# Kernel optimization log

Measured on AMD Instinct MI355X. Metric: run time of the kernel, lower is better.

Reference implementation:

```python
import jax, jax.numpy as jnp
import numpy as np
from jax import lax

B, C_IN, IMG, P, HID = 128, 3, 224, 16, 768
HW = (IMG // P) ** 2  # 196 patches


def setup_inputs() -> dict:
    key = jax.random.key(0)
    k1, k2, k3, k4 = jax.random.split(key, 4)
    x = jax.random.normal(k1, (B, C_IN, IMG, IMG), dtype=jnp.float32)
    # conv weight init scale ~ kaiming-ish, value irrelevant for correctness
    W = jax.random.normal(k2, (HID, C_IN, P, P), dtype=jnp.float32) * 0.02
    b = jax.random.normal(k3, (HID,), dtype=jnp.float32) * 0.02
    # per-sample random permutation of patch positions (the pixel shuffle)
    perm = jax.vmap(lambda k: jax.random.permutation(k, HW))(jax.random.split(k4, B)).astype(jnp.int32)
    return {"x": x, "W": W, "b": b, "perm": perm}


def reference(x, W, b, perm):
    # patchify conv: kernel_size == stride == P, no padding
    enc = lax.conv_general_dilated(
        x, W, window_strides=(P, P), padding="VALID",
        dimension_numbers=("NCHW", "OIHW", "NCHW"),
    ) + b[None, :, None, None]                      # [B, HID, H', W']
    Bc, Cc, Hc, Wc = enc.shape
    enc = enc.reshape(Bc, Cc, Hc * Wc).transpose(0, 2, 1)   # [B, HW, HID]
    # per-sample patch shuffle: shuffled[i, j] = enc[i, perm[i, j]]
    shuffled = jnp.take_along_axis(enc, perm[:, :, None], axis=1)
    return shuffled
```

## Files before the change

### kernel.cpp

```cpp
#include <hip/hip_runtime.h>
#include <hip/hip_bf16.h>

#define BATCH  128
#define HWN    196
#define HIDN   768
#define KN     768
#define IMGSZ  224
#define IMG2   (224*224)
#define MTOT   (BATCH*HWN)

#define BM 128
#define BN 128
#define BK 32
#define NBM (MTOT/BM)
#define NBN (HIDN/BN)
#define NWG (NBM*NBN)
#define CPX (NWG/8)

typedef __attribute__((ext_vector_type(8))) short bf16x8;
typedef __attribute__((ext_vector_type(4))) float floatx4;

#define GP(p) ((const __attribute__((address_space(1))) void*)(p))
#define SP(p) ((__attribute__((address_space(3))) void*)(p))

static __device__ __forceinline__ short f2bf(float f) {
    __hip_bfloat16 h = __float2bfloat16(f);
    return __builtin_bit_cast(short, h);
}

static __device__ __forceinline__ bf16x8 cvt8(const float* __restrict__ src) {
    float4 f0 = *(const float4*)(src);
    float4 f1 = *(const float4*)(src + 4);
    bf16x8 v;
    v[0]=f2bf(f0.x); v[1]=f2bf(f0.y); v[2]=f2bf(f0.z); v[3]=f2bf(f0.w);
    v[4]=f2bf(f1.x); v[5]=f2bf(f1.y); v[6]=f2bf(f1.z); v[7]=f2bf(f1.w);
    return v;
}

__global__ __launch_bounds__(256)
void prep_A(const float* __restrict__ x, unsigned short* __restrict__ A)
{
    const int idx = blockIdx.x * 256 + threadIdx.x;
    const int gr  = idx / 48;
    const int seg = idx - gr * 48;
    const int b   = gr / HWN;
    const int p   = gr - b * HWN;
    const int py  = p / 14, px = p - py * 14;
    const int c   = seg >> 4;
    const int iy  = seg & 15;

    const float* src = x + (size_t)b * 3 * IMG2 + (size_t)c * IMG2
                         + (size_t)(py * 16 + iy) * IMGSZ + px * 16;
    bf16x8 v0 = cvt8(src);
    bf16x8 v1 = cvt8(src + 8);
    unsigned short* dst = A + (size_t)gr * KN + seg * 16;
    *(bf16x8*)(dst)     = v0;
    *(bf16x8*)(dst + 8) = v1;
}

__global__ __launch_bounds__(256)
void prep_W(const float* __restrict__ W, unsigned short* __restrict__ Wb)
{
    const int idx = blockIdx.x * 256 + threadIdx.x;
    const float* src = W + (size_t)idx * 8;
    *(bf16x8*)(Wb + (size_t)idx * 8) = cvt8(src);
}

__global__ __launch_bounds__(256, 3)
void gemm(const unsigned short* __restrict__ A, const int* __restrict__ perm,
          const unsigned short* __restrict__ Wb,
          const float* __restrict__ bias, float* __restrict__ out)
{
    __shared__ __align__(16) unsigned short As[BM * BK];
    __shared__ __align__(16) unsigned short Bs[BN * BK];

    const int tid = threadIdx.x;
    const int wg  = blockIdx.x;
    const int lid = (wg & 7) * CPX + (wg >> 3);
    const int bm  = lid / NBN;
    const int bn  = lid - bm * NBN;

    const int srow = tid >> 2;
    const int sseg = tid & 3;
    const int gr0 = bm * BM + srow;
    const int gr1 = gr0 + 64;
    const int b0  = gr0 / HWN;
    const int b1  = gr1 / HWN;
    const int pr0 = b0 * HWN + perm[gr0];
    const int pr1 = b1 * HWN + perm[gr1];
    const unsigned short* ga0 = A  + (size_t)pr0 * KN + sseg * 8;
    const unsigned short* ga1 = A  + (size_t)pr1 * KN + sseg * 8;
    const unsigned short* gb  = Wb + (size_t)(bn * BN + srow) * KN + sseg * 8;

    const int lane = tid & 63;
    const int wave = tid >> 6;
    const int wm = (wave >> 1) * 64;
    const int wn = (wave & 1) * 64;
    const int lr = lane & 15;
    const int lq = lane >> 4;

    floatx4 acc[4][4] = {};

    for (int k0 = 0; k0 < KN; k0 += BK) {
        __builtin_amdgcn_global_load_lds(GP(ga0 + k0),           SP(&As[tid * 8]),        16, 0, 0);
        __builtin_amdgcn_global_load_lds(GP(ga1 + k0),           SP(&As[2048 + tid * 8]), 16, 0, 0);
        __builtin_amdgcn_global_load_lds(GP(gb + k0),            SP(&Bs[tid * 8]),        16, 0, 0);
        __builtin_amdgcn_global_load_lds(GP(gb + 64 * KN + k0),  SP(&Bs[2048 + tid * 8]), 16, 0, 0);
        __syncthreads();

        bf16x8 bfrag[4];
        #pragma unroll
        for (int j = 0; j < 4; ++j)
            bfrag[j] = *(const bf16x8*)&Bs[(wn + j * 16 + lr) * BK + lq * 8];
        #pragma unroll
        for (int i = 0; i < 4; ++i) {
            bf16x8 afrag = *(const bf16x8*)&As[(wm + i * 16 + lr) * BK + lq * 8];
            #pragma unroll
            for (int j = 0; j < 4; ++j)
                acc[i][j] = __builtin_amdgcn_mfma_f32_16x16x32_bf16(
                                afrag, bfrag[j], acc[i][j], 0, 0, 0);
        }
        __syncthreads();
    }

    #pragma unroll
    for (int j = 0; j < 4; ++j) {
        const int gc = bn * BN + wn + j * 16 + lr;
        const float bv = bias[gc];
        #pragma unroll
        for (int i = 0; i < 4; ++i) {
            const int grow = bm * BM + wm + i * 16 + lq * 4;
            float* op = out + (size_t)grow * HIDN + gc;
            #pragma unroll
            for (int r = 0; r < 4; ++r)
                op[(size_t)r * HIDN] = acc[i][j][r] + bv;
        }
    }
}

extern "C" void kernel_launch(void* const* d_in, const int* in_sizes, int n_in,
                              void* d_out, int out_size, void* d_ws, size_t ws_size,
                              hipStream_t stream) {
    const float* x    = (const float*)d_in[0];
    const float* W    = (const float*)d_in[1];
    const float* bias = (const float*)d_in[2];
    const int*   perm = (const int*)d_in[3];
    float* out = (float*)d_out;

    unsigned short* A  = (unsigned short*)d_ws;
    unsigned short* Wb = A + (size_t)MTOT * KN;

    prep_A<<<dim3(MTOT * 48 / 256), dim3(256), 0, stream>>>(x, A);
    prep_W<<<dim3(KN * HIDN / 8 / 256), dim3(256), 0, stream>>>(W, Wb);
    gemm<<<dim3(NWG), dim3(256), 0, stream>>>(A, perm, Wb, bias, out);
}
```

Measured before the change: 182.3 us.

## Double GEMM M-tile to 256 with 512 threads and fuse prep kernels

The GEMM workgroup grows to 512 threads covering a 256x128 output tile. The intent is to halve the number of times each B tile is reloaded and to let eight waves share the LDS-staged operands. The XCD swizzle is rewritten to handle a workgroup count that is not divisible by 8. The two bf16 conversion prep kernels are merged into one launch to save launch overhead. The larger tile leaves fewer workgroups (588) and raises LDS use per block, which may reduce occupancy and load balance.

```diff
diff --git a/kernel.cpp b/kernel.cpp
--- a/kernel.cpp
+++ b/kernel.cpp
@@ -9,13 +9,17 @@
 #define IMG2   (224*224)
 #define MTOT   (BATCH*HWN)
 
-#define BM 128
+#define BM 256
 #define BN 128
 #define BK 32
 #define NBM (MTOT/BM)
 #define NBN (HIDN/BN)
 #define NWG (NBM*NBN)
-#define CPX (NWG/8)
+#define SWQ (NWG/8)
+#define SWR (NWG%8)
+
+#define PWB (KN*HIDN/8/256)
+#define PAB (MTOT*48/256)
 
 typedef __attribute__((ext_vector_type(8))) short bf16x8;
 typedef __attribute__((ext_vector_type(4))) float floatx4;
@@ -38,9 +42,15 @@
 }
 
 __global__ __launch_bounds__(256)
-void prep_A(const float* __restrict__ x, unsigned short* __restrict__ A)
+void prep(const float* __restrict__ x, const float* __restrict__ W,
+          unsigned short* __restrict__ A, unsigned short* __restrict__ Wb)
 {
-    const int idx = blockIdx.x * 256 + threadIdx.x;
+    if (blockIdx.x < PWB) {
+        const int idx = blockIdx.x * 256 + threadIdx.x;
+        *(bf16x8*)(Wb + (size_t)idx * 8) = cvt8(W + (size_t)idx * 8);
+        return;
+    }
+    const int idx = (blockIdx.x - PWB) * 256 + threadIdx.x;
     const int gr  = idx / 48;
     const int seg = idx - gr * 48;
     const int b   = gr / HWN;
@@ -58,15 +68,7 @@
     *(bf16x8*)(dst + 8) = v1;
 }
 
-__global__ __launch_bounds__(256)
-void prep_W(const float* __restrict__ W, unsigned short* __restrict__ Wb)
-{
-    const int idx = blockIdx.x * 256 + threadIdx.x;
-    const float* src = W + (size_t)idx * 8;
-    *(bf16x8*)(Wb + (size_t)idx * 8) = cvt8(src);
-}
-
-__global__ __launch_bounds__(256, 3)
+__global__ __launch_bounds__(512, 6)
 void gemm(const unsigned short* __restrict__ A, const int* __restrict__ perm,
           const unsigned short* __restrict__ Wb,
           const float* __restrict__ bias, float* __restrict__ out)
@@ -76,18 +78,19 @@
 
     const int tid = threadIdx.x;
     const int wg  = blockIdx.x;
-    const int lid = (wg & 7) * CPX + (wg >> 3);
-    const int bm  = lid / NBN;
-    const int bn  = lid - bm * NBN;
+    const int xcd  = wg & 7;
+    const int slot = wg >> 3;
+    const int base = (xcd < SWR) ? xcd * (SWQ + 1) : SWR * (SWQ + 1) + (xcd - SWR) * SWQ;
+    const int lid  = base + slot;
+    const int bm   = lid / NBN;
+    const int bn   = lid - bm * NBN;
 
     const int srow = tid >> 2;
     const int sseg = tid & 3;
-    const int gr0 = bm * BM + srow;
-    const int gr1 = gr0 + 64;
-    const int b0  = gr0 / HWN;
-    const int b1  = gr1 / HWN;
-    const int pr0 = b0 * HWN + perm[gr0];
-    const int pr1 = b1 * HWN + perm[gr1];
+    const int gr0  = bm * BM + srow;
+    const int gr1  = gr0 + 128;
+    const int pr0  = (gr0 / HWN) * HWN + perm[gr0];
+    const int pr1  = (gr1 / HWN) * HWN + perm[gr1];
     const unsigned short* ga0 = A  + (size_t)pr0 * KN + sseg * 8;
     const unsigned short* ga1 = A  + (size_t)pr1 * KN + sseg * 8;
     const unsigned short* gb  = Wb + (size_t)(bn * BN + srow) * KN + sseg * 8;
@@ -102,10 +105,9 @@
     floatx4 acc[4][4] = {};
 
     for (int k0 = 0; k0 < KN; k0 += BK) {
-        __builtin_amdgcn_global_load_lds(GP(ga0 + k0),           SP(&As[tid * 8]),        16, 0, 0);
-        __builtin_amdgcn_global_load_lds(GP(ga1 + k0),           SP(&As[2048 + tid * 8]), 16, 0, 0);
-        __builtin_amdgcn_global_load_lds(GP(gb + k0),            SP(&Bs[tid * 8]),        16, 0, 0);
-        __builtin_amdgcn_global_load_lds(GP(gb + 64 * KN + k0),  SP(&Bs[2048 + tid * 8]), 16, 0, 0);
+        __builtin_amdgcn_global_load_lds(GP(ga0 + k0), SP(&As[tid * 8]),        16, 0, 0);
+        __builtin_amdgcn_global_load_lds(GP(ga1 + k0), SP(&As[4096 + tid * 8]), 16, 0, 0);
+        __builtin_amdgcn_global_load_lds(GP(gb  + k0), SP(&Bs[tid * 8]),        16, 0, 0);
         __syncthreads();
 
         bf16x8 bfrag[4];
@@ -150,7 +152,6 @@
     unsigned short* A  = (unsigned short*)d_ws;
     unsigned short* Wb = A + (size_t)MTOT * KN;
 
-    prep_A<<<dim3(MTOT * 48 / 256), dim3(256), 0, stream>>>(x, A);
-    prep_W<<<dim3(KN * HIDN / 8 / 256), dim3(256), 0, stream>>>(W, Wb);
-    gemm<<<dim3(NWG), dim3(256), 0, stream>>>(A, perm, Wb, bias, out);
+    prep<<<dim3(PWB + PAB), dim3(256), 0, stream>>>(x, W, A, Wb);
+    gemm<<<dim3(NWG), dim3(512), 0, stream>>>(A, perm, Wb, bias, out);
 }
```

Result: slower. 348.1 us (+91.0%).

## Double K tile with XOR-swizzled LDS and merge the two prep kernels

Applied to the files above, without the earlier changes.

Raises BK from 32 to 64, so each workgroup does half as many load/barrier iterations and runs two MFMA sub-steps per tile. The LDS layout gets an XOR swizzle on the 16-byte segments to avoid bank conflicts when reading 128-byte rows. The A and W conversion kernels are merged into one launch, and each A-conversion thread now handles two horizontally adjacent patches to save a launch and some index math. The cost is twice the LDS (32 KB per block), which may lower occupancy under the launch bound of 3 blocks.

```diff
diff --git a/kernel.cpp b/kernel.cpp
--- a/kernel.cpp
+++ b/kernel.cpp
@@ -11,11 +11,16 @@
 
 #define BM 128
 #define BN 128
-#define BK 32
+#define BK 64
+#define NT  (KN/BK)
 #define NBM (MTOT/BM)
 #define NBN (HIDN/BN)
 #define NWG (NBM*NBN)
 #define CPX (NWG/8)
+
+#define PWB   (KN*HIDN/8/256)
+#define NPAIR (MTOT/2)
+#define PAB   (NPAIR*48/256)
 
 typedef __attribute__((ext_vector_type(8))) short bf16x8;
 typedef __attribute__((ext_vector_type(4))) float floatx4;
@@ -38,32 +43,35 @@
 }
 
 __global__ __launch_bounds__(256)
-void prep_A(const float* __restrict__ x, unsigned short* __restrict__ A)
+void prep(const float* __restrict__ x, const float* __restrict__ W,
+          unsigned short* __restrict__ A, unsigned short* __restrict__ Wb)
 {
-    const int idx = blockIdx.x * 256 + threadIdx.x;
-    const int gr  = idx / 48;
-    const int seg = idx - gr * 48;
-    const int b   = gr / HWN;
-    const int p   = gr - b * HWN;
-    const int py  = p / 14, px = p - py * 14;
-    const int c   = seg >> 4;
-    const int iy  = seg & 15;
+    if (blockIdx.x < PWB) {
+        const int idx = blockIdx.x * 256 + threadIdx.x;
+        *(bf16x8*)(Wb + (size_t)idx * 8) = cvt8(W + (size_t)idx * 8);
+        return;
+    }
+    const int idx  = (blockIdx.x - PWB) * 256 + threadIdx.x;
+    const int pi   = idx / 48;
+    const int seg  = idx - pi * 48;
+    const int gr   = pi * 2;
+    const int b    = gr / HWN;
+    const int p    = gr - b * HWN;
+    const int py   = p / 14, px = p - py * 14;
+    const int c    = seg >> 4;
+    const int iy   = seg & 15;
 
     const float* src = x + (size_t)b * 3 * IMG2 + (size_t)c * IMG2
                          + (size_t)(py * 16 + iy) * IMGSZ + px * 16;
     bf16x8 v0 = cvt8(src);
     bf16x8 v1 = cvt8(src + 8);
-    unsigned short* dst = A + (size_t)gr * KN + seg * 16;
-    *(bf16x8*)(dst)     = v0;
-    *(bf16x8*)(dst + 8) = v1;
-}
-
-__global__ __launch_bounds__(256)
-void prep_W(const float* __restrict__ W, unsigned short* __restrict__ Wb)
-{
-    const int idx = blockIdx.x * 256 + threadIdx.x;
-    const float* src = W + (size_t)idx * 8;
-    *(bf16x8*)(Wb + (size_t)idx * 8) = cvt8(src);
+    bf16x8 v2 = cvt8(src + 16);
+    bf16x8 v3 = cvt8(src + 24);
+    unsigned short* d0 = A + (size_t)gr * KN + seg * 16;
+    *(bf16x8*)(d0)          = v0;
+    *(bf16x8*)(d0 + 8)      = v1;
+    *(bf16x8*)(d0 + KN)     = v2;
+    *(bf16x8*)(d0 + KN + 8) = v3;
 }
 
 __global__ __launch_bounds__(256, 3)
@@ -80,17 +88,19 @@
     const int bm  = lid / NBN;
     const int bn  = lid - bm * NBN;
 
-    const int srow = tid >> 2;
-    const int sseg = tid & 3;
-    const int gr0 = bm * BM + srow;
-    const int gr1 = gr0 + 64;
-    const int b0  = gr0 / HWN;
-    const int b1  = gr1 / HWN;
-    const int pr0 = b0 * HWN + perm[gr0];
-    const int pr1 = b1 * HWN + perm[gr1];
-    const unsigned short* ga0 = A  + (size_t)pr0 * KN + sseg * 8;
-    const unsigned short* ga1 = A  + (size_t)pr1 * KN + sseg * 8;
-    const unsigned short* gb  = Wb + (size_t)(bn * BN + srow) * KN + sseg * 8;
+    const int trow = tid >> 3;
+    const int xseg = (tid & 7) ^ (trow & 7);
+    const unsigned short* ga0; const unsigned short* ga1;
+    const unsigned short* ga2; const unsigned short* ga3;
+#define MKGA(PTR, G)                                                          \
+    do {                                                                      \
+        const int r  = bm * BM + (G) * 32 + trow;                             \
+        const int pr = (r / HWN) * HWN + perm[r];                             \
+        PTR = A + (size_t)pr * KN + xseg * 8;                                 \
+    } while (0)
+    MKGA(ga0, 0); MKGA(ga1, 1); MKGA(ga2, 2); MKGA(ga3, 3);
+#undef MKGA
+    const unsigned short* gb = Wb + (size_t)(bn * BN + trow) * KN + xseg * 8;
 
     const int lane = tid & 63;
     const int wave = tid >> 6;
@@ -98,27 +108,51 @@
     const int wn = (wave & 1) * 64;
     const int lr = lane & 15;
     const int lq = lane >> 4;
+    const int rx = (lr & 7) << 4;
+    const int rd0 = (lq * 16) ^ rx;
+    const int rd1 = ((64 + lq * 16)) ^ rx;
 
     floatx4 acc[4][4] = {};
 
-    for (int k0 = 0; k0 < KN; k0 += BK) {
-        __builtin_amdgcn_global_load_lds(GP(ga0 + k0),           SP(&As[tid * 8]),        16, 0, 0);
-        __builtin_amdgcn_global_load_lds(GP(ga1 + k0),           SP(&As[2048 + tid * 8]), 16, 0, 0);
-        __builtin_amdgcn_global_load_lds(GP(gb + k0),            SP(&Bs[tid * 8]),        16, 0, 0);
-        __builtin_amdgcn_global_load_lds(GP(gb + 64 * KN + k0),  SP(&Bs[2048 + tid * 8]), 16, 0, 0);
+    for (int it = 0; it < NT; ++it) {
+        const int k0 = it * BK;
+        __builtin_amdgcn_global_load_lds(GP(ga0 + k0),          SP(&As[tid * 8]),        16, 0, 0);
+        __builtin_amdgcn_global_load_lds(GP(ga1 + k0),          SP(&As[2048 + tid * 8]), 16, 0, 0);
+        __builtin_amdgcn_global_load_lds(GP(ga2 + k0),          SP(&As[4096 + tid * 8]), 16, 0, 0);
+        __builtin_amdgcn_global_load_lds(GP(ga3 + k0),          SP(&As[6144 + tid * 8]), 16, 0, 0);
+        __builtin_amdgcn_global_load_lds(GP(gb + k0),           SP(&Bs[tid * 8]),        16, 0, 0);
+        __builtin_amdgcn_global_load_lds(GP(gb + 32 * KN + k0), SP(&Bs[2048 + tid * 8]), 16, 0, 0);
+        __builtin_amdgcn_global_load_lds(GP(gb + 64 * KN + k0), SP(&Bs[4096 + tid * 8]), 16, 0, 0);
+        __builtin_amdgcn_global_load_lds(GP(gb + 96 * KN + k0), SP(&Bs[6144 + tid * 8]), 16, 0, 0);
         __syncthreads();
 
-        bf16x8 bfrag[4];
-        #pragma unroll
-        for (int j = 0; j < 4; ++j)
-            bfrag[j] = *(const bf16x8*)&Bs[(wn + j * 16 + lr) * BK + lq * 8];
-        #pragma unroll
-        for (int i = 0; i < 4; ++i) {
-            bf16x8 afrag = *(const bf16x8*)&As[(wm + i * 16 + lr) * BK + lq * 8];
+        {
+            bf16x8 bfrag[4];
             #pragma unroll
             for (int j = 0; j < 4; ++j)
-                acc[i][j] = __builtin_amdgcn_mfma_f32_16x16x32_bf16(
-                                afrag, bfrag[j], acc[i][j], 0, 0, 0);
+                bfrag[j] = *(const bf16x8*)((const char*)Bs + (wn + j * 16 + lr) * 128 + rd0);
+            #pragma unroll
+            for (int i = 0; i < 4; ++i) {
+                const bf16x8 afrag = *(const bf16x8*)((const char*)As + (wm + i * 16 + lr) * 128 + rd0);
+                #pragma unroll
+                for (int j = 0; j < 4; ++j)
+                    acc[i][j] = __builtin_amdgcn_mfma_f32_16x16x32_bf16(
+                                    afrag, bfrag[j], acc[i][j], 0, 0, 0);
+            }
+        }
+        {
+            bf16x8 bfrag[4];
+            #pragma unroll
+            for (int j = 0; j < 4; ++j)
+                bfrag[j] = *(const bf16x8*)((const char*)Bs + (wn + j * 16 + lr) * 128 + rd1);
+            #pragma unroll
+            for (int i = 0; i < 4; ++i) {
+                const bf16x8 afrag = *(const bf16x8*)((const char*)As + (wm + i * 16 + lr) * 128 + rd1);
+                #pragma unroll
+                for (int j = 0; j < 4; ++j)
+                    acc[i][j] = __builtin_amdgcn_mfma_f32_16x16x32_bf16(
+                                    afrag, bfrag[j], acc[i][j], 0, 0, 0);
+            }
         }
         __syncthreads();
     }
@@ -150,7 +184,6 @@
     unsigned short* A  = (unsigned short*)d_ws;
     unsigned short* Wb = A + (size_t)MTOT * KN;
 
-    prep_A<<<dim3(MTOT * 48 / 256), dim3(256), 0, stream>>>(x, A);
-    prep_W<<<dim3(KN * HIDN / 8 / 256), dim3(256), 0, stream>>>(W, Wb);
+    prep<<<dim3(PWB + PAB), dim3(256), 0, stream>>>(x, W, A, Wb);
     gemm<<<dim3(NWG), dim3(256), 0, stream>>>(A, perm, Wb, bias, out);
 }
```

After: 184.2 us. No clear change (+1.0%).
